# Performance work log

Hardware: AMD Instinct MI355X
Metric: run time of the kernel (lower is better)

Reference implementation:

```python
import jax, jax.numpy as jnp
import numpy as np


def _lstm(x_seq, W, U, b, h0, c0):
    """Keras-default LSTM. x_seq: [B,T,F]. Gate order i,f,g,o.
    Returns (all hidden states [B,T,H], final h [B,H], final c [B,H])."""
    H = U.shape[0]
    # precompute input projections for all timesteps: [T,B,4H]
    xz = jnp.einsum('btf,fg->tbg', x_seq, W) + b

    def step(carry, xz_t):
        h, c = carry
        z = xz_t + h @ U  # [B,4H]
        i = jax.nn.sigmoid(z[:, 0 * H:1 * H])
        f = jax.nn.sigmoid(z[:, 1 * H:2 * H])
        g = jnp.tanh(z[:, 2 * H:3 * H])
        o = jax.nn.sigmoid(z[:, 3 * H:4 * H])
        c = f * c + i * g
        h = o * jnp.tanh(c)
        return (h, c), h

    (hT, cT), hs = jax.lax.scan(step, (h0, c0), xz)
    return jnp.transpose(hs, (1, 0, 2)), hT, cT  # [B,T,H], [B,H], [B,H]


def setup_inputs() -> dict:
    key = jax.random.key(0)
    ks = jax.random.split(key, 7)
    B, T, F, H, C = 128, 512, 128, 512, 10
    s_in1 = 1.0 / np.sqrt(F)
    s_h = 1.0 / np.sqrt(H)
    return {
        'x': jax.random.normal(ks[0], (B, T, F), jnp.float32),
        'W1': jax.random.normal(ks[1], (F, 4 * H), jnp.float32) * s_in1,
        'U1': jax.random.normal(ks[2], (H, 4 * H), jnp.float32) * s_h,
        'b1': jnp.zeros((4 * H,), jnp.float32),
        'W2': jax.random.normal(ks[3], (H, 4 * H), jnp.float32) * s_h,
        'U2': jax.random.normal(ks[4], (H, 4 * H), jnp.float32) * s_h,
        'b2': jnp.zeros((4 * H,), jnp.float32),
        'Wd': jax.random.normal(ks[5], (H, C), jnp.float32) * s_h,
        'bd': jnp.zeros((C,), jnp.float32),
    }


def reference(x, W1, U1, b1, W2, U2, b2, Wd, bd):
    B = x.shape[0]
    H = U1.shape[0]
    h0 = jnp.zeros((B, H), x.dtype)
    c0 = jnp.zeros((B, H), x.dtype)
    # lstm1: return_sequences + return_state
    seq, h1, c1 = _lstm(x, W1, U1, b1, h0, c0)
    # Keras RNN called on [seq, h, c] uses (h, c) as lstm2's initial state
    _, h2, _ = _lstm(seq, W2, U2, b2, h1, c1)
    logits = h2 @ Wd + bd
    return jax.nn.softmax(logits, axis=-1)
```

## Files before the change

### kernel.cpp

```cpp
#include <hip/hip_runtime.h>
#include <math.h>

#define BB 128
#define TT 512
#define FF 128
#define HH 512
#define NR 2048
#define HB (HH*BB)
#define FLS 16

typedef __attribute__((ext_vector_type(8))) short short8;
typedef __attribute__((ext_vector_type(4))) float f32x4;
typedef unsigned int uint;
typedef unsigned short ushort;
typedef unsigned long long u64;

#define MFMA __builtin_amdgcn_mfma_f32_16x16x32_bf16
#define AT_LD(p)   __hip_atomic_load((p), __ATOMIC_RELAXED, __HIP_MEMORY_SCOPE_AGENT)
#define AT_ST(p,v) __hip_atomic_store((p), (v), __ATOMIC_RELAXED, __HIP_MEMORY_SCOPE_AGENT)
#define PLD(p)     (*(p))

__device__ __forceinline__ ushort f2bf(float f) {
  uint u = __float_as_uint(f);
  u += 0x7fff + ((u >> 16) & 1);
  return (ushort)(u >> 16);
}
__device__ __forceinline__ float bfh(ushort h) { return __uint_as_float(((uint)h) << 16); }
__device__ __forceinline__ u64 pk2f(float a, float b) {
  return ((u64)__float_as_uint(b) << 32) | (u64)__float_as_uint(a);
}
__device__ __forceinline__ float ftanh(float v) {
  float t = __expf(2.f * v);
  return 1.f - 2.f / (t + 1.f);
}
__device__ __forceinline__ void split8(const uint* w, short8& bh, short8& bl) {
  union { short8 v; uint d[4]; } H, Lo;
#pragma unroll
  for (int d = 0; d < 4; ++d) {
    H.d[d]  = __builtin_amdgcn_perm(w[2 * d + 1], w[2 * d], 0x07060302u);
    Lo.d[d] = __builtin_amdgcn_perm(w[2 * d + 1], w[2 * d], 0x05040100u);
  }
  bh = H.v; bl = Lo.v;
}


__global__ __launch_bounds__(256) void k_zero(float* __restrict__ p, int n) {
  int i = blockIdx.x * 256 + threadIdx.x;
  if (i < n) p[i] = 0.f;
}

__global__ __launch_bounds__(256) void k_rearr_b(const float* __restrict__ src,
                                                 float* __restrict__ dst) {
  int idx = blockIdx.x * 256 + threadIdx.x;
  int j = idx & 511, g = idx >> 9;
  dst[j * 4 + g] = src[idx];
}

__global__ __launch_bounds__(256) void k_pack_A(const float* __restrict__ src,
                                                ushort* __restrict__ dst, int ktsh) {
  int idx = blockIdx.x * 256 + threadIdx.x;
  int KTm1 = (1 << ktsh) - 1;
  int j8 = idx & 7;
  int L = (idx >> 3) & 63;
  int kt = (idx >> 9) & KTm1;
  int jb = idx >> (9 + ktsh);
  int k = kt * 32 + (L >> 4) * 8 + j8;
  int m = L & 15;
  int j = jb * 4 + (m >> 2);
  int g = m & 3;
  float v = src[(size_t)k * NR + g * HH + j];
  ushort hi = f2bf(v);
  ushort lo = f2bf(v - bfh(hi));
  size_t base = ((size_t)((jb << ktsh) + kt) * 64 + L) * 16;
  dst[base + j8] = hi;
  dst[base + 8 + j8] = lo;
}

__global__ __launch_bounds__(256, 1) void k_fused(
    const float* __restrict__ x,
    const ushort* __restrict__ W1pk, const ushort* __restrict__ U1pk,
    const float* __restrict__ bp1,
    const ushort* __restrict__ W2pk, const ushort* __restrict__ U2pk,
    const float* __restrict__ bp2,
    uint* __restrict__ seq, uint* __restrict__ ring,
    float4* __restrict__ xzr,
    int* __restrict__ hflags, int* __restrict__ pflags) {
  int tid = threadIdx.x;
  int L = tid & 63;
  int w = tid >> 6;
  int q = L >> 4, n = L & 15;
  int h = w & 1, p = w >> 1;
  bool isrec = (blockIdx.x < 128);
  int b = isrec ? blockIdx.x : (blockIdx.x - 128);
  int ch = b & 3, jb4 = b >> 2;
  int rt0 = jb4 * 4 + 2 * p;
  int jbp_own = rt0 + h;
  int j_own = jbp_own * 4 + q;
  int col0 = ch * 32 + n;
  int pidx = b * FLS;
  int rgive = 2 * p + 1 - h;
  int rkeep = 2 * p + h;

  __shared__ f32x4 xch[4][2][64];

  short8 uh[2][8], ul[2][8];

#define LOADMM(HS, LD, COLC, ZP) {                                       \
    uint wv[8][8];                                                       \
    const uint* hc = (HS) + (size_t)(q * 8) * BB + (COLC);               \
    _Pragma("unroll")                                                    \
    for (int kk = 0; kk < 8; ++kk)                                       \
      _Pragma("unroll")                                                  \
      for (int u = 0; u < 8; ++u)                                        \
        wv[kk][u] = LD(hc + (size_t)(kk * 32 + u) * BB);                 \
    f32x4 A0[2], A1[2], A2[2];                                           \
    _Pragma("unroll")                                                    \
    for (int r = 0; r < 2; ++r) {                                        \
      A0[r] = (f32x4){0.f, 0.f, 0.f, 0.f}; A1[r] = A0[r]; A2[r] = A0[r]; \
    }                                                                    \
    _Pragma("unroll")                                                    \
    for (int kk = 0; kk < 8; ++kk) {                                     \
      short8 bh, bl;                                                     \
      split8(wv[kk], bh, bl);                                            \
      _Pragma("unroll")                                                  \
      for (int r = 0; r < 2; ++r) {                                      \
        A0[r] = MFMA(uh[r][kk], bh, A0[r], 0, 0, 0);                     \
        A1[r] = MFMA(ul[r][kk], bh, A1[r], 0, 0, 0);                     \
        A2[r] = MFMA(uh[r][kk], bl, A2[r], 0, 0, 0);                     \
      }                                                                  \
    }                                                                    \
    ZP[0] = A0[0] + A1[0] + A2[0];                                       \
    ZP[1] = A0[1] + A1[1] + A2[1];                                       \
  }

#define ACT(ZV, X0, X1, X2, X3, CREF, WORD) {                            \
    float z0_ = (ZV).x + (X0), z1_ = (ZV).y + (X1);                      \
    float z2_ = (ZV).z + (X2), z3_ = (ZV).w + (X3);                      \
    float ig = 1.f / (1.f + __expf(-z0_));                               \
    float fg = 1.f / (1.f + __expf(-z1_));                               \
    float gg = ftanh(z2_);                                               \
    float og = 1.f / (1.f + __expf(-z3_));                               \
    (CREF) = fg * (CREF) + ig * gg;                                      \
    float hn = og * ftanh(CREF);                                         \
    ushort hh = f2bf(hn);                                                \
    (WORD) = (((uint)hh) << 16) | (uint)f2bf(hn - bfh(hh));              \
  }

  if (isrec) {
#pragma unroll
    for (int r = 0; r < 2; ++r)
#pragma unroll
      for (int kk = 0; kk < 8; ++kk) {
        const ushort* pp = U1pk + (((size_t)(rt0 + r) * 16 + (8 * h + kk)) * 64 + L) * 16;
        uh[r][kk] = *(const short8*)(pp); ul[r][kk] = *(const short8*)(pp + 8);
      }
    float c0 = 0.f, c1 = 0.f;
    int fidx = ((16 * h + (L & 15)) * 4 + ch) * FLS;

#pragma unroll 1
    for (int G = 0; G < 2 * TT; ++G) {
      if (G == TT) {
#pragma unroll
        for (int r = 0; r < 2; ++r)
#pragma unroll
          for (int kk = 0; kk < 8; ++kk) {
            const ushort* pp = U2pk + (((size_t)(rt0 + r) * 16 + (8 * h + kk)) * 64 + L) * 16;
            uh[r][kk] = *(const short8*)(pp); ul[r][kk] = *(const short8*)(pp + 8);
          }
      }
      while (true) {
        int hf = AT_LD(hflags + fidx);
        int pf = AT_LD(pflags + pidx);
        if (__all((hf >= G) && (pf >= G + 1))) break;
      }
      asm volatile("" ::: "memory");
      const u64* xpa = (const u64*)(xzr + ((size_t)(G & 7) * HB + (size_t)j_own * BB + col0));
      const u64* xpb = (const u64*)(xzr + ((size_t)(G & 7) * HB + (size_t)j_own * BB + col0 + 16));
      u64 qa0 = AT_LD(xpa), qa1 = AT_LD(xpa + 1);
      u64 qb0 = AT_LD(xpb), qb1 = AT_LD(xpb + 1);

      f32x4 zp0[2], zp1[2];
      if (G != 0) {
        if (G < TT) {
          const uint* hs = seq + (size_t)(G - 1) * HB + (size_t)(256 * h) * BB;
          LOADMM(hs, PLD, col0, zp0);
          LOADMM(hs, PLD, col0 + 16, zp1);
        } else {
          const uint* hs = ring + (size_t)((G - 1) & 3) * HB + (size_t)(256 * h) * BB;
          LOADMM(hs, AT_LD, col0, zp0);
          LOADMM(hs, AT_LD, col0 + 16, zp1);
        }
      } else {
        zp0[0] = (f32x4){0.f, 0.f, 0.f, 0.f}; zp0[1] = zp0[0];
        zp1[0] = zp0[0]; zp1[1] = zp0[0];
      }
      xch[rgive][0][L] = h ? zp0[0] : zp0[1];
      xch[rgive][1][L] = h ? zp1[0] : zp1[1];
      __syncthreads();
      f32x4 z0 = (h ? zp0[1] : zp0[0]) + xch[rkeep][0][L];
      f32x4 z1 = (h ? zp1[1] : zp1[0]) + xch[rkeep][1][L];

      uint wd0, wd1;
      ACT(z0, __uint_as_float((uint)qa0), __uint_as_float((uint)(qa0 >> 32)),
          __uint_as_float((uint)qa1), __uint_as_float((uint)(qa1 >> 32)), c0, wd0);
      ACT(z1, __uint_as_float((uint)qb0), __uint_as_float((uint)(qb0 >> 32)),
          __uint_as_float((uint)qb1), __uint_as_float((uint)(qb1 >> 32)), c1, wd1);

      if (G < TT) {
        AT_ST(&seq[(size_t)G * HB + (size_t)j_own * BB + col0], wd0);
        AT_ST(&seq[(size_t)G * HB + (size_t)j_own * BB + col0 + 16], wd1);
        if (G == TT - 1) {
          AT_ST(&ring[(size_t)3 * HB + (size_t)j_own * BB + col0], wd0);
          AT_ST(&ring[(size_t)3 * HB + (size_t)j_own * BB + col0 + 16], wd1);
        }
      } else {
        AT_ST(&ring[(size_t)(G & 3) * HB + (size_t)j_own * BB + col0], wd0);
        AT_ST(&ring[(size_t)(G & 3) * HB + (size_t)j_own * BB + col0 + 16], wd1);
      }
      __syncthreads();
      if (tid == 0) AT_ST(hflags + pidx, G + 1);
    }
  } else {
#pragma unroll
    for (int r = 0; r < 2; ++r)
#pragma unroll
      for (int kk = 0; kk < 2; ++kk) {
        const ushort* pp = W1pk + (((size_t)(rt0 + r) * 4 + (2 * h + kk)) * 64 + L) * 16;
        uh[r][kk] = *(const short8*)(pp); ul[r][kk] = *(const short8*)(pp + 8);
      }
    float4 bv = *(const float4*)(bp1 + j_own * 4);

#pragma unroll 1
    for (int G = 0; G < 2 * TT; ++G) {
      if (G == TT) {
#pragma unroll
        for (int r = 0; r < 2; ++r)
#pragma unroll
          for (int kk = 0; kk < 8; ++kk) {
            const ushort* pp = W2pk + (((size_t)(rt0 + r) * 16 + (8 * h + kk)) * 64 + L) * 16;
            uh[r][kk] = *(const short8*)(pp); ul[r][kk] = *(const short8*)(pp + 8);
          }
        bv = *(const float4*)(bp2 + j_own * 4);
      }
      if (G >= 8) {
        while (AT_LD(hflags + pidx) < G - 7) __builtin_amdgcn_s_sleep(1);
      }
      asm volatile("" ::: "memory");

      f32x4 zp0[2], zp1[2];
      if (G < TT) {
#pragma unroll
        for (int r = 0; r < 2; ++r) {
          zp0[r] = (f32x4){0.f, 0.f, 0.f, 0.f}; zp1[r] = zp0[r];
        }
#define PROJA_CT(COLC, ZP) {                                             \
        f32x4 P0[2], P1[2], P2[2];                                       \
        _Pragma("unroll")                                                \
        for (int r = 0; r < 2; ++r) {                                    \
          P0[r] = (f32x4){0.f, 0.f, 0.f, 0.f}; P1[r] = P0[r]; P2[r] = P0[r]; \
        }                                                                \
        const float* xp = x + ((size_t)(COLC) * TT + G) * FF + q * 8 + 64 * h; \
        _Pragma("unroll")                                                \
        for (int kk = 0; kk < 2; ++kk) {                                 \
          float4 v0 = *(const float4*)(xp + kk * 32);                    \
          float4 v1 = *(const float4*)(xp + kk * 32 + 4);                \
          float xf[8] = {v0.x, v0.y, v0.z, v0.w, v1.x, v1.y, v1.z, v1.w}; \
          short8 xh, xl;                                                 \
          _Pragma("unroll")                                              \
          for (int u = 0; u < 8; ++u) {                                  \
            ushort hi = f2bf(xf[u]);                                     \
            xl[u] = (short)f2bf(xf[u] - bfh(hi));                        \
            xh[u] = (short)hi;                                           \
          }                                                              \
          _Pragma("unroll")                                              \
          for (int r = 0; r < 2; ++r) {                                  \
            P0[r] = MFMA(uh[r][kk], xh, P0[r], 0, 0, 0);                 \
            P1[r] = MFMA(ul[r][kk], xh, P1[r], 0, 0, 0);                 \
            P2[r] = MFMA(uh[r][kk], xl, P2[r], 0, 0, 0);                 \
          }                                                              \
        }                                                                \
        ZP[0] = P0[0] + P1[0] + P2[0];                                   \
        ZP[1] = P0[1] + P1[1] + P2[1];                                   \
      }
        PROJA_CT(col0, zp0);
        PROJA_CT(col0 + 16, zp1);
      } else {
        int sp = G - TT;
        const uint* hs = seq + (size_t)sp * HB + (size_t)(256 * h) * BB;
        LOADMM(hs, PLD, col0, zp0);
        LOADMM(hs, PLD, col0 + 16, zp1);
      }
      xch[rgive][0][L] = h ? zp0[0] : zp0[1];
      xch[rgive][1][L] = h ? zp1[0] : zp1[1];
      __syncthreads();
      f32x4 z0 = (h ? zp0[1] : zp0[0]) + xch[rkeep][0][L];
      f32x4 z1 = (h ? zp1[1] : zp1[0]) + xch[rkeep][1][L];
      {
        u64* dp = (u64*)(xzr + ((size_t)(G & 7) * HB + (size_t)j_own * BB + col0));
        AT_ST(dp, pk2f(z0.x + bv.x, z0.y + bv.y));
        AT_ST(dp + 1, pk2f(z0.z + bv.z, z0.w + bv.w));
        u64* dq = (u64*)(xzr + ((size_t)(G & 7) * HB + (size_t)j_own * BB + col0 + 16));
        AT_ST(dq, pk2f(z1.x + bv.x, z1.y + bv.y));
        AT_ST(dq + 1, pk2f(z1.z + bv.z, z1.w + bv.w));
      }
      __syncthreads();
      if (tid == 0) AT_ST(pflags + pidx, G + 1);
    }
  }
}

__global__ __launch_bounds__(64) void k_dense(const uint* __restrict__ h2,
                                              const float* __restrict__ Wd,
                                              const float* __restrict__ bd,
                                              float* __restrict__ out) {
  int b = blockIdx.x * 64 + threadIdx.x;
  float acc[10];
#pragma unroll
  for (int c = 0; c < 10; ++c) acc[c] = bd[c];
  for (int k = 0; k < HH; ++k) {
    uint w = h2[k * BB + b];
    float hv = __uint_as_float(w & 0xffff0000u) + __uint_as_float(w << 16);
#pragma unroll
    for (int c = 0; c < 10; ++c) acc[c] = fmaf(hv, Wd[k * 10 + c], acc[c]);
  }
  float m = acc[0];
#pragma unroll
  for (int c = 1; c < 10; ++c) m = fmaxf(m, acc[c]);
  float s = 0.f;
#pragma unroll
  for (int c = 0; c < 10; ++c) { acc[c] = __expf(acc[c] - m); s += acc[c]; }
  float inv = 1.f / s;
#pragma unroll
  for (int c = 0; c < 10; ++c) out[b * 10 + c] = acc[c] * inv;
}

extern "C" void kernel_launch(void* const* d_in, const int* in_sizes, int n_in,
                              void* d_out, int out_size, void* d_ws, size_t ws_size,
                              hipStream_t stream) {
  const float* x  = (const float*)d_in[0];
  const float* W1 = (const float*)d_in[1];
  const float* U1 = (const float*)d_in[2];
  const float* b1 = (const float*)d_in[3];
  const float* W2 = (const float*)d_in[4];
  const float* U2 = (const float*)d_in[5];
  const float* b2 = (const float*)d_in[6];
  const float* Wd = (const float*)d_in[7];
  const float* bd = (const float*)d_in[8];
  float* out = (float*)d_out;

  uint*   seq   = (uint*)d_ws;
  uint*   ring  = seq + (size_t)TT * HB;
  float4* xzr   = (float4*)(ring + (size_t)4 * HB);
  ushort* W1pk  = (ushort*)(xzr + (size_t)8 * HB);
  ushort* U1pk  = W1pk + (size_t)524288;
  ushort* U2pk  = U1pk + (size_t)2097152;
  ushort* W2pk  = U2pk + (size_t)2097152;
  float*  bp1   = (float*)(W2pk + (size_t)2097152);
  float*  bp2   = bp1 + NR;
  int*    hflags = (int*)(bp2 + NR);
  int*    pflags = hflags + 128 * FLS;

  k_zero<<<16, 256, 0, stream>>>((float*)hflags, 2 * 128 * FLS);
  k_rearr_b<<<8, 256, 0, stream>>>(b1, bp1);
  k_rearr_b<<<8, 256, 0, stream>>>(b2, bp2);
  k_pack_A<<<1024, 256, 0, stream>>>(W1, W1pk, 2);
  k_pack_A<<<4096, 256, 0, stream>>>(U1, U1pk, 4);
  k_pack_A<<<4096, 256, 0, stream>>>(U2, U2pk, 4);
  k_pack_A<<<4096, 256, 0, stream>>>(W2, W2pk, 4);

  k_fused<<<256, 256, 0, stream>>>(x, W1pk, U1pk, bp1, W2pk, U2pk, bp2,
                                   seq, ring, xzr, hflags, pflags);
  k_dense<<<2, 64, 0, stream>>>(ring + (size_t)3 * HB, Wd, bd, out);
}
```

Before: 5.206 ms.

## Transpose LSTM2 hidden-state ring to batch-major and pin weight registers

The ring buffer holding layer-2 hidden states now uses a batch-major layout, so each lane reads eight contiguous words with 64-bit atomic loads instead of 64 strided 32-bit atomic loads. The producer stores and the final dense kernel are changed to match the new layout. Empty inline asm constraints pin the preloaded weight fragments in VGPRs, to stop the compiler from rematerialising or spilling them. The transposed stores become strided and uncoalesced, and the dense kernel's reads lose coalescing across threads.

```diff
diff --git a/kernel.cpp b/kernel.cpp
--- a/kernel.cpp
+++ b/kernel.cpp
@@ -19,6 +19,7 @@
 #define AT_LD(p)   __hip_atomic_load((p), __ATOMIC_RELAXED, __HIP_MEMORY_SCOPE_AGENT)
 #define AT_ST(p,v) __hip_atomic_store((p), (v), __ATOMIC_RELAXED, __HIP_MEMORY_SCOPE_AGENT)
 #define PLD(p)     (*(p))
+#define PIN8(v)    asm volatile("" : "+v"(v))
 
 __device__ __forceinline__ ushort f2bf(float f) {
   uint u = __float_as_uint(f);
@@ -105,14 +106,14 @@
 
   short8 uh[2][8], ul[2][8];
 
-#define LOADMM(HS, LD, COLC, ZP) {                                       \
+#define LOADMM(HS, COLC, ZP) {                                           \
     uint wv[8][8];                                                       \
     const uint* hc = (HS) + (size_t)(q * 8) * BB + (COLC);               \
     _Pragma("unroll")                                                    \
     for (int kk = 0; kk < 8; ++kk)                                       \
       _Pragma("unroll")                                                  \
       for (int u = 0; u < 8; ++u)                                        \
-        wv[kk][u] = LD(hc + (size_t)(kk * 32 + u) * BB);                 \
+        wv[kk][u] = PLD(hc + (size_t)(kk * 32 + u) * BB);                \
     f32x4 A0[2], A1[2], A2[2];                                           \
     _Pragma("unroll")                                                    \
     for (int r = 0; r < 2; ++r) {                                        \
@@ -133,6 +134,41 @@
     ZP[1] = A0[1] + A1[1] + A2[1];                                       \
   }
 
+#define LOADMM_T(SLOT, COLC, ZP) {                                       \
+    u64 wq[8][4];                                                        \
+    const u64* hc = (const u64*)(ring + (size_t)(SLOT) * HB              \
+                    + (size_t)(COLC) * HH + 256 * h + q * 8);            \
+    _Pragma("unroll")                                                    \
+    for (int kk = 0; kk < 8; ++kk)                                       \
+      _Pragma("unroll")                                                  \
+      for (int u4 = 0; u4 < 4; ++u4)                                     \
+        wq[kk][u4] = AT_LD(hc + kk * 16 + u4);                           \
+    f32x4 A0[2], A1[2], A2[2];                                           \
+    _Pragma("unroll")                                                    \
+    for (int r = 0; r < 2; ++r) {                                        \
+      A0[r] = (f32x4){0.f, 0.f, 0.f, 0.f}; A1[r] = A0[r]; A2[r] = A0[r]; \
+    }                                                                    \
+    _Pragma("unroll")                                                    \
+    for (int kk = 0; kk < 8; ++kk) {                                     \
+      uint wv8[8];                                                       \
+      _Pragma("unroll")                                                  \
+      for (int u4 = 0; u4 < 4; ++u4) {                                   \
+        wv8[2 * u4]     = (uint)wq[kk][u4];                              \
+        wv8[2 * u4 + 1] = (uint)(wq[kk][u4] >> 32);                      \
+      }                                                                  \
+      short8 bh, bl;                                                     \
+      split8(wv8, bh, bl);                                               \
+      _Pragma("unroll")                                                  \
+      for (int r = 0; r < 2; ++r) {                                      \
+        A0[r] = MFMA(uh[r][kk], bh, A0[r], 0, 0, 0);                     \
+        A1[r] = MFMA(ul[r][kk], bh, A1[r], 0, 0, 0);                     \
+        A2[r] = MFMA(uh[r][kk], bl, A2[r], 0, 0, 0);                     \
+      }                                                                  \
+    }                                                                    \
+    ZP[0] = A0[0] + A1[0] + A2[0];                                       \
+    ZP[1] = A0[1] + A1[1] + A2[1];                                       \
+  }
+
 #define ACT(ZV, X0, X1, X2, X3, CREF, WORD) {                            \
     float z0_ = (ZV).x + (X0), z1_ = (ZV).y + (X1);                      \
     float z2_ = (ZV).z + (X2), z3_ = (ZV).w + (X3);                      \
@@ -146,6 +182,10 @@
     (WORD) = (((uint)hh) << 16) | (uint)f2bf(hn - bfh(hh));              \
   }
 
+#define PIN_ALL() { _Pragma("unroll") for (int r = 0; r < 2; ++r)        \
+    _Pragma("unroll") for (int kk = 0; kk < 8; ++kk) {                   \
+      PIN8(uh[r][kk]); PIN8(ul[r][kk]); } }
+
   if (isrec) {
 #pragma unroll
     for (int r = 0; r < 2; ++r)
@@ -154,6 +194,7 @@
         const ushort* pp = U1pk + (((size_t)(rt0 + r) * 16 + (8 * h + kk)) * 64 + L) * 16;
         uh[r][kk] = *(const short8*)(pp); ul[r][kk] = *(const short8*)(pp + 8);
       }
+    PIN_ALL();
     float c0 = 0.f, c1 = 0.f;
     int fidx = ((16 * h + (L & 15)) * 4 + ch) * FLS;
 
@@ -167,6 +208,7 @@
             const ushort* pp = U2pk + (((size_t)(rt0 + r) * 16 + (8 * h + kk)) * 64 + L) * 16;
             uh[r][kk] = *(const short8*)(pp); ul[r][kk] = *(const short8*)(pp + 8);
           }
+        PIN_ALL();
       }
       while (true) {
         int hf = AT_LD(hflags + fidx);
@@ -183,12 +225,12 @@
       if (G != 0) {
         if (G < TT) {
           const uint* hs = seq + (size_t)(G - 1) * HB + (size_t)(256 * h) * BB;
-          LOADMM(hs, PLD, col0, zp0);
-          LOADMM(hs, PLD, col0 + 16, zp1);
+          LOADMM(hs, col0, zp0);
+          LOADMM(hs, col0 + 16, zp1);
         } else {
-          const uint* hs = ring + (size_t)((G - 1) & 3) * HB + (size_t)(256 * h) * BB;
-          LOADMM(hs, AT_LD, col0, zp0);
-          LOADMM(hs, AT_LD, col0 + 16, zp1);
+          int slot = (G - 1) & 3;
+          LOADMM_T(slot, col0, zp0);
+          LOADMM_T(slot, col0 + 16, zp1);
         }
       } else {
         zp0[0] = (f32x4){0.f, 0.f, 0.f, 0.f}; zp0[1] = zp0[0];
@@ -210,12 +252,12 @@
         AT_ST(&seq[(size_t)G * HB + (size_t)j_own * BB + col0], wd0);
         AT_ST(&seq[(size_t)G * HB + (size_t)j_own * BB + col0 + 16], wd1);
         if (G == TT - 1) {
-          AT_ST(&ring[(size_t)3 * HB + (size_t)j_own * BB + col0], wd0);
-          AT_ST(&ring[(size_t)3 * HB + (size_t)j_own * BB + col0 + 16], wd1);
+          AT_ST(&ring[(size_t)3 * HB + (size_t)col0 * HH + j_own], wd0);
+          AT_ST(&ring[(size_t)3 * HB + (size_t)(col0 + 16) * HH + j_own], wd1);
         }
       } else {
-        AT_ST(&ring[(size_t)(G & 3) * HB + (size_t)j_own * BB + col0], wd0);
-        AT_ST(&ring[(size_t)(G & 3) * HB + (size_t)j_own * BB + col0 + 16], wd1);
+        AT_ST(&ring[(size_t)(G & 3) * HB + (size_t)col0 * HH + j_own], wd0);
+        AT_ST(&ring[(size_t)(G & 3) * HB + (size_t)(col0 + 16) * HH + j_own], wd1);
       }
       __syncthreads();
       if (tid == 0) AT_ST(hflags + pidx, G + 1);
@@ -240,6 +282,7 @@
             const ushort* pp = W2pk + (((size_t)(rt0 + r) * 16 + (8 * h + kk)) * 64 + L) * 16;
             uh[r][kk] = *(const short8*)(pp); ul[r][kk] = *(const short8*)(pp + 8);
           }
+        PIN_ALL();
         bv = *(const float4*)(bp2 + j_own * 4);
       }
       if (G >= 8) {
@@ -287,8 +330,8 @@
       } else {
         int sp = G - TT;
         const uint* hs = seq + (size_t)sp * HB + (size_t)(256 * h) * BB;
-        LOADMM(hs, PLD, col0, zp0);
-        LOADMM(hs, PLD, col0 + 16, zp1);
+        LOADMM(hs, col0, zp0);
+        LOADMM(hs, col0 + 16, zp1);
       }
       xch[rgive][0][L] = h ? zp0[0] : zp0[1];
       xch[rgive][1][L] = h ? zp1[0] : zp1[1];
@@ -318,7 +361,7 @@
 #pragma unroll
   for (int c = 0; c < 10; ++c) acc[c] = bd[c];
   for (int k = 0; k < HH; ++k) {
-    uint w = h2[k * BB + b];
+    uint w = h2[(size_t)b * HH + k];
     float hv = __uint_as_float(w & 0xffff0000u) + __uint_as_float(w << 16);
 #pragma unroll
     for (int c = 0; c < 10; ++c) acc[c] = fmaf(hv, Wd[k * 10 + c], acc[c]);
```

Measured after the change: 7.223 ms. 1.39x slower.
